# Optimization experiments

Measured on AMD Instinct MI355X. Metric: run time of the kernel, lower is better.

Reference implementation:

```python
import jax, jax.numpy as jnp
import numpy as np

N_GENES = 3072
N_CELLS = 3072
HIDDEN = 64
CAUSAL = 16
CS = 32
ALPHA = 0.35  # LeakyReLU negative slope
NEG_BIG = -9.0e15


def setup_inputs() -> dict:
    key = jax.random.key(0)
    ks = jax.random.split(key, 20)
    s = 0.05
    return {
        "x": jax.random.normal(ks[0], (N_CELLS, N_GENES), jnp.float32),
        "adj": jax.random.randint(ks[1], (N_GENES, N_GENES), 0, 2, jnp.int32),
        "eps": jax.random.normal(ks[2], (N_GENES, CAUSAL), jnp.float32),
        "W_gat": jax.random.normal(ks[3], (N_CELLS, HIDDEN), jnp.float32) * s,
        "a_gat": jax.random.normal(ks[4], (2 * HIDDEN,), jnp.float32) * s,
        "W_mu": jax.random.normal(ks[5], (HIDDEN, CAUSAL), jnp.float32) * s,
        "b_mu": jnp.zeros((CAUSAL,), jnp.float32),
        "W_lv": jax.random.normal(ks[6], (HIDDEN, CAUSAL), jnp.float32) * s,
        "b_lv": jnp.zeros((CAUSAL,), jnp.float32),
        "W_diff": jax.random.normal(ks[7], (CAUSAL + HIDDEN, CS), jnp.float32) * s,
        "b_diff": jnp.zeros((CS,), jnp.float32),
        "W_dec": jax.random.normal(ks[8], (CS, N_CELLS), jnp.float32) * s,
        "b_dec": jnp.zeros((N_CELLS,), jnp.float32),
        "W_gcn1": jax.random.normal(ks[9], (N_CELLS, HIDDEN), jnp.float32) * s,
        "W_gcn2": jax.random.normal(ks[10], (HIDDEN, HIDDEN), jnp.float32) * s,
    }


def _gcn(xg, adjf, W):
    # adj + I, symmetric normalization D^-1/2 A D^-1/2, then A_norm @ (x @ W), relu
    A = adjf + jnp.eye(adjf.shape[0], dtype=adjf.dtype)
    d = A.sum(axis=1)
    d_inv_sqrt = jnp.where(d > 0, d ** -0.5, 0.0)
    A_norm = d_inv_sqrt[:, None] * A * d_inv_sqrt[None, :]
    return jax.nn.relu(A_norm @ (xg @ W))


def reference(x, adj, eps, W_gat, a_gat, W_mu, b_mu, W_lv, b_lv,
              W_diff, b_diff, W_dec, b_dec, W_gcn1, W_gcn2):
    adjf = adj.astype(jnp.float32)
    # ---- GAT layer (batch of 1, squeezed). h: (M, F)
    h = x.T @ W_gat
    F = h.shape[1]
    # a_input[i, j] = concat(h_j, h_i)  => e_ij = leakyrelu(a1.h_j + a2.h_i)
    s_dst = h @ a_gat[:F]   # contribution of column index j
    s_src = h @ a_gat[F:]   # contribution of row index i
    e = jax.nn.leaky_relu(s_src[:, None] + s_dst[None, :], ALPHA)
    e = jnp.where(adjf > 0, e, NEG_BIG)
    att = jax.nn.softmax(e, axis=1)  # dropout p=0.1 is identity in eval mode
    h_gat = jax.nn.elu(att @ h)      # (M, HIDDEN)
    # ---- causal VAE encode + reparameterize
    mu = h_gat @ W_mu + b_mu
    logvar = h_gat @ W_lv + b_lv
    z = mu + eps * jnp.exp(0.5 * logvar)
    # ---- diffusion fusion
    cs = jax.nn.relu(jnp.concatenate([z, h_gat], axis=-1) @ W_diff + b_diff)
    # ---- decoder
    x_recon = jax.nn.sigmoid(cs @ W_dec + b_dec)  # (M, N_CELLS)
    # ---- inference model (two GCN layers on x_recon.T, as in original code)
    h1 = _gcn(x_recon.T, adjf, W_gcn1)
    h2 = _gcn(h1, adjf, W_gcn2)
    ie = jnp.concatenate([h2, cs], axis=-1)
    return (x_recon, h2, ie, cs, mu, logvar)
```

## Files before the change

kernel.cpp:

```cpp
#include <hip/hip_runtime.h>
#include <math.h>

#define N 3072
#define H 64
#define CAUS 16
#define CSD 32
#define GAT_ALPHA 0.35f
#define SLICES 8
#define JSL (N / SLICES)
#define MMS 16
#define JMM (N / MMS)
#define NH (N * H)
typedef unsigned long long u64;
typedef unsigned short u16;
typedef __attribute__((ext_vector_type(4))) float f32x4;
typedef __attribute__((ext_vector_type(8))) short s16x8;
struct alignas(8) u16x4 { u16 x, y, z, w; };
struct T4 { float4 r[4]; };

__device__ inline u16 f2bf(float f) {
  unsigned u = __builtin_bit_cast(unsigned, f);
  u += 0x7fffu + ((u >> 16) & 1u);
  return (u16)(u >> 16);
}

__device__ inline T4 t_load(const float* __restrict__ src, int ld, int t) {
  int k4 = (t >> 4) * 4, m4 = (t & 15) * 4;
  T4 o;
#pragma unroll
  for (int d = 0; d < 4; d++)
    o.r[d] = *(const float4*)(src + (size_t)(k4 + d) * ld + m4);
  return o;
}
__device__ inline void t_store(u16 (&dst)[64][72], const T4& v, int t) {
  int k4 = (t >> 4) * 4, m4 = (t & 15) * 4;
  u16x4 c0 = {f2bf(v.r[0].x), f2bf(v.r[1].x), f2bf(v.r[2].x), f2bf(v.r[3].x)};
  u16x4 c1 = {f2bf(v.r[0].y), f2bf(v.r[1].y), f2bf(v.r[2].y), f2bf(v.r[3].y)};
  u16x4 c2 = {f2bf(v.r[0].z), f2bf(v.r[1].z), f2bf(v.r[2].z), f2bf(v.r[3].z)};
  u16x4 c3 = {f2bf(v.r[0].w), f2bf(v.r[1].w), f2bf(v.r[2].w), f2bf(v.r[3].w)};
  *(u16x4*)&dst[m4 + 0][k4] = c0;
  *(u16x4*)&dst[m4 + 1][k4] = c1;
  *(u16x4*)&dst[m4 + 2][k4] = c2;
  *(u16x4*)&dst[m4 + 3][k4] = c3;
}

__global__ __launch_bounds__(256) void k_pack(const int* __restrict__ adj,
                                              u64* __restrict__ packed,
                                              float* __restrict__ dis) {
  int row = blockIdx.x * 4 + (threadIdx.x >> 6);
  int lane = threadIdx.x & 63;
  const int* ar = adj + (size_t)row * N;
  int deg = 0;
  for (int w0 = 0; w0 < 48; w0 += 8) {
    int vals[8];
#pragma unroll
    for (int q = 0; q < 8; q++) vals[q] = ar[(w0 + q) * 64 + lane];
#pragma unroll
    for (int q = 0; q < 8; q++) {
      u64 m = __ballot(vals[q] > 0);
      if (lane == 0) packed[(size_t)row * 48 + w0 + q] = m;
      deg += (vals[q] > 0) ? 1 : 0;
    }
  }
  for (int off = 32; off; off >>= 1) deg += __shfl_xor(deg, off);
  if (lane == 0) dis[row] = rsqrtf((float)deg + 1.0f);
}

__global__ __launch_bounds__(256) void k_mm32(const float* __restrict__ A, int lda,
                                              const float* __restrict__ B, int ldb,
                                              float* __restrict__ outp) {
  __shared__ u16 As[32][72];
  __shared__ u16 Bs[64][72];
  int t = threadIdx.x;
  int g0 = blockIdx.x * 32;
  int c0 = blockIdx.y * JMM;
  int w = t >> 6, l = t & 63, il = l & 15, kg = l >> 4;
  int ri = w & 1, cj = w >> 1;
  int ak = (t >> 3) * 2, am = (t & 7) * 4;
  f32x4 acc0 = {0.f, 0.f, 0.f, 0.f}, acc1 = {0.f, 0.f, 0.f, 0.f};
  float4 a0 = *(const float4*)(A + (size_t)(c0 + ak) * lda + g0 + am);
  float4 a1 = *(const float4*)(A + (size_t)(c0 + ak + 1) * lda + g0 + am);
  T4 bv = t_load(B + (size_t)c0 * ldb, ldb, t);
  for (int cb = 0; cb < JMM; cb += 64) {
    __syncthreads();
    As[am + 0][ak] = f2bf(a0.x); As[am + 1][ak] = f2bf(a0.y);
    As[am + 2][ak] = f2bf(a0.z); As[am + 3][ak] = f2bf(a0.w);
    As[am + 0][ak + 1] = f2bf(a1.x); As[am + 1][ak + 1] = f2bf(a1.y);
    As[am + 2][ak + 1] = f2bf(a1.z); As[am + 3][ak + 1] = f2bf(a1.w);
    t_store(Bs, bv, t);
    if (cb + 64 < JMM) {
      a0 = *(const float4*)(A + (size_t)(c0 + cb + 64 + ak) * lda + g0 + am);
      a1 = *(const float4*)(A + (size_t)(c0 + cb + 65 + ak) * lda + g0 + am);
      bv = t_load(B + (size_t)(c0 + cb + 64) * ldb, ldb, t);
    }
    __syncthreads();
#pragma unroll
    for (int kk = 0; kk < 64; kk += 32) {
      s16x8 a = *(const s16x8*)&As[ri * 16 + il][kk + kg * 8];
      s16x8 b0 = *(const s16x8*)&Bs[cj * 32 + il][kk + kg * 8];
      s16x8 b1 = *(const s16x8*)&Bs[cj * 32 + 16 + il][kk + kg * 8];
      acc0 = __builtin_amdgcn_mfma_f32_16x16x32_bf16(a, b0, acc0, 0, 0, 0);
      acc1 = __builtin_amdgcn_mfma_f32_16x16x32_bf16(a, b1, acc1, 0, 0, 0);
    }
  }
  float* ob = outp + (size_t)blockIdx.y * NH;
#pragma unroll
  for (int c = 0; c < 2; c++) {
    f32x4 acc = c ? acc1 : acc0;
    int col = cj * 32 + c * 16 + il;
    int rbase = g0 + ri * 16 + kg * 4;
#pragma unroll
    for (int r = 0; r < 4; r++)
      ob[(size_t)(rbase + r) * H + col] = acc[r];
  }
}

template <int GAT>
__global__ __launch_bounds__(256) void k_agg(const float* __restrict__ hin,
                                             const u64* __restrict__ packed,
                                             const float* __restrict__ sdst,
                                             const float* __restrict__ ssrc,
                                             const float* __restrict__ dis,
                                             float* __restrict__ outp,
                                             float* __restrict__ zpart) {
  __shared__ u16 Ws[32][72];
  __shared__ u16 Hs[64][72];
  __shared__ float ssl[32];
  int t = threadIdx.x;
  int i0 = blockIdx.x * 32;
  int jbase = blockIdx.y * JSL;
  int w = t >> 6, l = t & 63, il = l & 15, kg = l >> 4;
  int ri = w & 1, cj = w >> 1;
  int r = t >> 3, jq = (t & 7) * 8;
  if (GAT && t < 32) ssl[t] = ssrc[i0 + t];
  __syncthreads();
  float sv = GAT ? ssl[r] : 0.f;
  float zacc = 0.f;
  f32x4 acc0 = {0.f, 0.f, 0.f, 0.f}, acc1 = {0.f, 0.f, 0.f, 0.f};

  auto gen_w = [&](int j0, float (&wv)[8]) {
    u64 wb = packed[(size_t)(i0 + r) * 48 + (j0 >> 6)];
    if (GAT) {
      const float4* s4p = (const float4*)(sdst + j0 + jq);
      float4 s0 = s4p[0], s1 = s4p[1];
      float sf[8] = {s0.x, s0.y, s0.z, s0.w, s1.x, s1.y, s1.z, s1.w};
#pragma unroll
      for (int q = 0; q < 8; q++) {
        float e = sv + sf[q];
        e = e > 0.f ? e : GAT_ALPHA * e;
        float ww = ((wb >> (jq + q)) & 1ULL) ? __expf(e) : 0.f;
        wv[q] = ww;
        zacc += ww;
      }
    } else {
      const float4* d4p = (const float4*)(dis + j0 + jq);
      float4 d0 = d4p[0], d1 = d4p[1];
      float df[8] = {d0.x, d0.y, d0.z, d0.w, d1.x, d1.y, d1.z, d1.w};
#pragma unroll
      for (int q = 0; q < 8; q++) {
        float cnt = (float)((wb >> (jq + q)) & 1ULL) +
                    ((i0 + r) == (j0 + jq + q) ? 1.f : 0.f);
        wv[q] = cnt * df[q];
      }
    }
  };

  T4 hv = t_load(hin + (size_t)jbase * H, H, t);
  float wv[8];
  gen_w(jbase, wv);
  for (int jb = 0; jb < JSL; jb += 64) {
    __syncthreads();
    t_store(Hs, hv, t);
    u16x4 w0 = {f2bf(wv[0]), f2bf(wv[1]), f2bf(wv[2]), f2bf(wv[3])};
    u16x4 w1 = {f2bf(wv[4]), f2bf(wv[5]), f2bf(wv[6]), f2bf(wv[7])};
    *(u16x4*)&Ws[r][jq] = w0;
    *(u16x4*)&Ws[r][jq + 4] = w1;
    if (jb + 64 < JSL) {
      hv = t_load(hin + (size_t)(jbase + jb + 64) * H, H, t);
      gen_w(jbase + jb + 64, wv);
    }
    __syncthreads();
#pragma unroll
    for (int kk = 0; kk < 64; kk += 32) {
      s16x8 a = *(const s16x8*)&Ws[ri * 16 + il][kk + kg * 8];
      s16x8 b0 = *(const s16x8*)&Hs[cj * 32 + il][kk + kg * 8];
      s16x8 b1 = *(const s16x8*)&Hs[cj * 32 + 16 + il][kk + kg * 8];
      acc0 = __builtin_amdgcn_mfma_f32_16x16x32_bf16(a, b0, acc0, 0, 0, 0);
      acc1 = __builtin_amdgcn_mfma_f32_16x16x32_bf16(a, b1, acc1, 0, 0, 0);
    }
  }
  if (GAT) {
    zacc += __shfl_xor(zacc, 1);
    zacc += __shfl_xor(zacc, 2);
    zacc += __shfl_xor(zacc, 4);
    if ((t & 7) == 0) zpart[(size_t)blockIdx.y * N + i0 + r] = zacc;
  }
  float* ob = outp + (size_t)blockIdx.y * NH;
#pragma unroll
  for (int c = 0; c < 2; c++) {
    f32x4 acc = c ? acc1 : acc0;
    int col = cj * 32 + c * 16 + il;
    int rbase = i0 + ri * 16 + kg * 4;
#pragma unroll
    for (int rr = 0; rr < 4; rr++)
      ob[(size_t)(rbase + rr) * H + col] = acc[rr];
  }
}

__global__ __launch_bounds__(256) void k_mmdec32(const float* __restrict__ cs,
                                                 const float* __restrict__ Wdec,
                                                 const float* __restrict__ bdec,
                                                 const float* __restrict__ Wg1,
                                                 float* __restrict__ xr,
                                                 float* __restrict__ outp) {
  __shared__ u16 As[32][72];
  __shared__ u16 Bs[64][72];
  __shared__ u16 Wd[32][40];
  __shared__ u16 Csh[64][40];
  __shared__ float bs_s[32];
  int t = threadIdx.x;
  int g0 = blockIdx.x * 32;
  int c0 = blockIdx.y * JSL;
  int w = t >> 6, l = t & 63, il = l & 15, kg = l >> 4;
  int ri = w & 1, cj = w >> 1;
  {
    int q = t >> 3, m4 = (t & 7) * 4;
    float4 v = *(const float4*)(Wdec + (size_t)q * N + g0 + m4);
    Wd[m4 + 0][q] = f2bf(v.x); Wd[m4 + 1][q] = f2bf(v.y);
    Wd[m4 + 2][q] = f2bf(v.z); Wd[m4 + 3][q] = f2bf(v.w);
    if (t < 32) bs_s[t] = bdec[g0 + t];
  }
  int cell = t >> 3, qf = (t & 7) * 4;
  float4 cv0 = *(const float4*)(cs + (size_t)(c0 + cell) * CSD + qf);
  float4 cv1 = *(const float4*)(cs + (size_t)(c0 + 32 + cell) * CSD + qf);
  T4 bv = t_load(Wg1 + (size_t)c0 * H, H, t);
  f32x4 z = {0.f, 0.f, 0.f, 0.f};
  f32x4 acc0 = z, acc1 = z;
  for (int cb = 0; cb < JSL; cb += 64) {
    __syncthreads();
    u16x4 u0 = {f2bf(cv0.x), f2bf(cv0.y), f2bf(cv0.z), f2bf(cv0.w)};
    u16x4 u1 = {f2bf(cv1.x), f2bf(cv1.y), f2bf(cv1.z), f2bf(cv1.w)};
    *(u16x4*)&Csh[cell][qf] = u0;
    *(u16x4*)&Csh[cell + 32][qf] = u1;
    t_store(Bs, bv, t);
    if (cb + 64 < JSL) {
      cv0 = *(const float4*)(cs + (size_t)(c0 + cb + 64 + cell) * CSD + qf);
      cv1 = *(const float4*)(cs + (size_t)(c0 + cb + 96 + cell) * CSD + qf);
      bv = t_load(Wg1 + (size_t)(c0 + cb + 64) * H, H, t);
    }
    __syncthreads();
    f32x4 dec0 = z, dec1 = z;
    {
      s16x8 a = *(const s16x8*)&Wd[ri * 16 + il][kg * 8];
      s16x8 b0 = *(const s16x8*)&Csh[cj * 32 + il][kg * 8];
      s16x8 b1 = *(const s16x8*)&Csh[cj * 32 + 16 + il][kg * 8];
      dec0 = __builtin_amdgcn_mfma_f32_16x16x32_bf16(a, b0, dec0, 0, 0, 0);
      dec1 = __builtin_amdgcn_mfma_f32_16x16x32_bf16(a, b1, dec1, 0, 0, 0);
    }
#pragma unroll
    for (int c = 0; c < 2; c++) {
      f32x4 dv = c ? dec1 : dec0;
      int kcol = cj * 32 + c * 16 + il;
      int mb = ri * 16 + kg * 4;
      float4 sv4;
      float* sp = (float*)&sv4;
#pragma unroll
      for (int r = 0; r < 4; r++) {
        float pre = dv[r] + bs_s[mb + r];
        float sg = 1.f / (1.f + __expf(-pre));
        sp[r] = sg;
        As[mb + r][kcol] = f2bf(sg);
      }
      *(float4*)(xr + (size_t)(c0 + cb + kcol) * N + g0 + mb) = sv4;
    }
    __syncthreads();
#pragma unroll
    for (int kk = 0; kk < 64; kk += 32) {
      s16x8 a = *(const s16x8*)&As[ri * 16 + il][kk + kg * 8];
      s16x8 b0 = *(const s16x8*)&Bs[cj * 32 + il][kk + kg * 8];
      s16x8 b1 = *(const s16x8*)&Bs[cj * 32 + 16 + il][kk + kg * 8];
      acc0 = __builtin_amdgcn_mfma_f32_16x16x32_bf16(a, b0, acc0, 0, 0, 0);
      acc1 = __builtin_amdgcn_mfma_f32_16x16x32_bf16(a, b1, acc1, 0, 0, 0);
    }
  }
  float* ob = outp + (size_t)blockIdx.y * NH;
#pragma unroll
  for (int c = 0; c < 2; c++) {
    f32x4 acc = c ? acc1 : acc0;
    int col = cj * 32 + c * 16 + il;
    int rbase = g0 + ri * 16 + kg * 4;
#pragma unroll
    for (int r = 0; r < 4; r++)
      ob[(size_t)(rbase + r) * H + col] = acc[r];
  }
}

__global__ __launch_bounds__(256) void k_reduce_sd(const float* __restrict__ src,
                                                   const float* __restrict__ a,
                                                   float* __restrict__ h,
                                                   float* __restrict__ sdst,
                                                   float* __restrict__ ssrc) {
  int row = blockIdx.x * 4 + (threadIdx.x >> 6);
  int lane = threadIdx.x & 63;
  size_t off = (size_t)row * H + lane;
  float v = 0.f;
#pragma unroll
  for (int p = 0; p < MMS; p++) v += src[(size_t)p * NH + off];
  h[off] = v;
  float d1 = v * a[lane];
  float d2 = v * a[H + lane];
  for (int o = 32; o; o >>= 1) {
    d1 += __shfl_xor(d1, o);
    d2 += __shfl_xor(d2, o);
  }
  if (lane == 0) { sdst[row] = d1; ssrc[row] = d2; }
}

__global__ __launch_bounds__(256) void k_reduce(const float4* __restrict__ src,
                                                float4* __restrict__ dst) {
  int idx = blockIdx.x * 256 + threadIdx.x;
  float4 v = {0, 0, 0, 0};
#pragma unroll
  for (int p = 0; p < SLICES; p++) {
    float4 u = src[(size_t)p * (NH / 4) + idx];
    v.x += u.x; v.y += u.y; v.z += u.z; v.w += u.w;
  }
  dst[idx] = v;
}

__global__ __launch_bounds__(256) void k_vae(const float* __restrict__ hacc,
                                             const float* __restrict__ zpart,
                                             const float* __restrict__ eps,
                                             const float* __restrict__ Wmu,
                                             const float* __restrict__ bmu,
                                             const float* __restrict__ Wlv,
                                             const float* __restrict__ blv,
                                             const float* __restrict__ Wd,
                                             const float* __restrict__ bd,
                                             float* __restrict__ mu_o,
                                             float* __restrict__ lv_o,
                                             float* __restrict__ cs_o,
                                             float* __restrict__ ie) {
  __shared__ float hs[16][65];
  __shared__ float zs[16][17];
  __shared__ float wmu_s[1024];
  __shared__ float wlv_s[1024];
  __shared__ float wd_s[2560];
  int t = threadIdx.x;
  int row0 = blockIdx.x * 16;
  {
    int rr = t >> 4, pp = t & 15;
    float zv = (pp < SLICES) ? zpart[(size_t)pp * N + row0 + rr] : 0.f;
    zv += __shfl_xor(zv, 1);
    zv += __shfl_xor(zv, 2);
    zv += __shfl_xor(zv, 4);
    zv += __shfl_xor(zv, 8);
    float zi = 1.0f / fmaxf(zv, 1e-30f);
    const float4* g4 = (const float4*)(hacc + (size_t)row0 * H);
    float4 v = {0, 0, 0, 0};
#pragma unroll
    for (int p = 0; p < SLICES; p++) {
      float4 u = g4[(size_t)p * (NH / 4) + t];
      v.x += u.x; v.y += u.y; v.z += u.z; v.w += u.w;
    }
    int c0 = (t & 15) * 4;
    float e0 = v.x * zi, e1 = v.y * zi, e2 = v.z * zi, e3 = v.w * zi;
    hs[rr][c0 + 0] = e0 > 0.f ? e0 : __expf(e0) - 1.f;
    hs[rr][c0 + 1] = e1 > 0.f ? e1 : __expf(e1) - 1.f;
    hs[rr][c0 + 2] = e2 > 0.f ? e2 : __expf(e2) - 1.f;
    hs[rr][c0 + 3] = e3 > 0.f ? e3 : __expf(e3) - 1.f;
  }
#pragma unroll
  for (int k = 0; k < 4; k++) {
    int lin = t + k * 256;
    wmu_s[lin] = Wmu[lin];
    wlv_s[lin] = Wlv[lin];
  }
#pragma unroll
  for (int k = 0; k < 10; k++) {
    int lin = t + k * 256;
    wd_s[lin] = Wd[lin];
  }
  __syncthreads();
  int r = t >> 4, kk = t & 15;
  float mu = bmu[kk], lv = blv[kk];
#pragma unroll 8
  for (int l = 0; l < 64; l++) {
    float hv = hs[r][l];
    mu += hv * wmu_s[l * 16 + kk];
    lv += hv * wlv_s[l * 16 + kk];
  }
  float zc = mu + eps[(size_t)(row0 + r) * CAUS + kk] * __expf(0.5f * lv);
  mu_o[(size_t)(row0 + r) * CAUS + kk] = mu;
  lv_o[(size_t)(row0 + r) * CAUS + kk] = lv;
  zs[r][kk] = zc;
  __syncthreads();
#pragma unroll
  for (int p = 0; p < 2; p++) {
    int lin = t + p * 256;
    int rr = lin >> 5, c = lin & 31;
    float acc = bd[c];
#pragma unroll 4
    for (int q = 0; q < 16; q++) acc += zs[rr][q] * wd_s[q * 32 + c];
#pragma unroll 8
    for (int l = 0; l < 64; l++) acc += hs[rr][l] * wd_s[(16 + l) * 32 + c];
    float v = fmaxf(acc, 0.f);
    cs_o[(size_t)(row0 + rr) * CSD + c] = v;
    ie[(size_t)(row0 + rr) * 96 + 64 + c] = v;
  }
}

__global__ __launch_bounds__(256) void k_h1w2(const float* __restrict__ h1src,
                                              const float* __restrict__ dis,
                                              const float* __restrict__ W2,
                                              float* __restrict__ t2) {
  __shared__ float w2s[64 * 64];
  __shared__ float hs[4][65];
  int t = threadIdx.x;
  int row0 = blockIdx.x * 4;
#pragma unroll
  for (int k = 0; k < 16; k++) w2s[t + k * 256] = W2[t + k * 256];
  {
    int rr = t >> 6;
    size_t off = (size_t)row0 * H + t;
    float v = 0.f;
#pragma unroll
    for (int p = 0; p < SLICES; p++) v += h1src[(size_t)p * NH + off];
    hs[rr][t & 63] = fmaxf(v * dis[row0 + rr], 0.f);
  }
  __syncthreads();
  int r = t >> 6, f = t & 63;
  float acc = 0.f;
#pragma unroll 8
  for (int l = 0; l < 64; l++) acc += hs[r][l] * w2s[l * 64 + f];
  t2[(size_t)(row0 + r) * H + f] = acc;
}

__global__ __launch_bounds__(256) void k_fin2(const float* __restrict__ h2src,
                                              const float* __restrict__ dis,
                                              float* __restrict__ h2,
                                              float* __restrict__ ie) {
  int idx = blockIdx.x * 256 + threadIdx.x;
  int row = idx >> 6, f = idx & 63;
  float v = 0.f;
#pragma unroll
  for (int p = 0; p < SLICES; p++) v += h2src[(size_t)p * NH + idx];
  v = fmaxf(v * dis[row], 0.f);
  h2[idx] = v;
  ie[(size_t)row * 96 + f] = v;
}

extern "C" void kernel_launch(void* const* d_in, const int* in_sizes, int n_in,
                              void* d_out, int out_size, void* d_ws, size_t ws_size,
                              hipStream_t stream) {
  const float* x    = (const float*)d_in[0];
  const int*   adj  = (const int*)d_in[1];
  const float* eps  = (const float*)d_in[2];
  const float* Wgat = (const float*)d_in[3];
  const float* agat = (const float*)d_in[4];
  const float* Wmu  = (const float*)d_in[5];
  const float* bmu  = (const float*)d_in[6];
  const float* Wlv  = (const float*)d_in[7];
  const float* blv  = (const float*)d_in[8];
  const float* Wdif = (const float*)d_in[9];
  const float* bdif = (const float*)d_in[10];
  const float* Wdec = (const float*)d_in[11];
  const float* bdec = (const float*)d_in[12];
  const float* Wg1  = (const float*)d_in[13];
  const float* Wg2  = (const float*)d_in[14];

  float* out = (float*)d_out;
  float* xr  = out;
  float* h2  = out + 9437184;
  float* ie  = out + 9633792;
  float* cs  = out + 9928704;
  float* muo = out + 10027008;
  float* lvo = out + 10076160;

  u64* packed = (u64*)d_ws;
  float* wf    = (float*)d_ws + 294912;
  float* part  = wf;
  float* h     = part + (size_t)MMS * NH;
  float* t1    = h + NH;
  float* t2    = t1 + NH;
  float* sdst  = t2 + NH;
  float* ssrc  = sdst + N;
  float* dis   = ssrc + N;
  float* zpart = dis + N;

  k_mm32<<<dim3(96, MMS), 256, 0, stream>>>(x, N, Wgat, H, part);
  k_pack<<<768, 256, 0, stream>>>(adj, packed, dis);
  k_reduce_sd<<<768, 256, 0, stream>>>(part, agat, h, sdst, ssrc);
  k_agg<1><<<dim3(96, SLICES), 256, 0, stream>>>(h, packed, sdst, ssrc, dis,
                                                 part, zpart);
  k_vae<<<192, 256, 0, stream>>>(part, zpart, eps, Wmu, bmu, Wlv, blv,
                                 Wdif, bdif, muo, lvo, cs, ie);
  k_mmdec32<<<dim3(96, SLICES), 256, 0, stream>>>(cs, Wdec, bdec, Wg1, xr, part);
  k_reduce<<<192, 256, 0, stream>>>((const float4*)part, (float4*)t1);
  k_agg<0><<<dim3(96, SLICES), 256, 0, stream>>>(t1, packed, nullptr, nullptr,
                                                 dis, part, nullptr);
  k_h1w2<<<768, 256, 0, stream>>>(part, dis, Wg2, t2);
  k_agg<0><<<dim3(96, SLICES), 256, 0, stream>>>(t2, packed, nullptr, nullptr,
                                                 dis, part, nullptr);
  k_fin2<<<768, 256, 0, stream>>>(part, dis, h2, ie);
}
```

Baseline: 100.5 us.

## Fuse GAT projection with adjacency packing and split decoder over more slices

Merges the x^T@W_gat matmul and the adjacency bit-packing into one launch. Extra blocks beyond 1536 do the packing, which saves a launch and lets the two independent stages run at the same time. Both the matmul and the decoder kernel now load all three 64-deep K chunks up front instead of double-buffering one chunk. The decoder is split into 16 slices instead of 8, which gives it more blocks but doubles the partial buffers that k_reduce must sum. Together these raise register pressure and partial-sum traffic in exchange for more memory-level parallelism.

```diff
diff --git a/kernel.cpp b/kernel.cpp
--- a/kernel.cpp
+++ b/kernel.cpp
@@ -44,55 +44,56 @@
   *(u16x4*)&dst[m4 + 3][k4] = c3;
 }
 
-__global__ __launch_bounds__(256) void k_pack(const int* __restrict__ adj,
+__global__ __launch_bounds__(256) void k_mmpk(const float* __restrict__ x,
+                                              const float* __restrict__ Wgat,
+                                              float* __restrict__ part,
+                                              const int* __restrict__ adj,
                                               u64* __restrict__ packed,
                                               float* __restrict__ dis) {
-  int row = blockIdx.x * 4 + (threadIdx.x >> 6);
-  int lane = threadIdx.x & 63;
-  const int* ar = adj + (size_t)row * N;
-  int deg = 0;
-  for (int w0 = 0; w0 < 48; w0 += 8) {
-    int vals[8];
-#pragma unroll
-    for (int q = 0; q < 8; q++) vals[q] = ar[(w0 + q) * 64 + lane];
-#pragma unroll
-    for (int q = 0; q < 8; q++) {
-      u64 m = __ballot(vals[q] > 0);
-      if (lane == 0) packed[(size_t)row * 48 + w0 + q] = m;
-      deg += (vals[q] > 0) ? 1 : 0;
-    }
-  }
-  for (int off = 32; off; off >>= 1) deg += __shfl_xor(deg, off);
-  if (lane == 0) dis[row] = rsqrtf((float)deg + 1.0f);
-}
-
-__global__ __launch_bounds__(256) void k_mm32(const float* __restrict__ A, int lda,
-                                              const float* __restrict__ B, int ldb,
-                                              float* __restrict__ outp) {
   __shared__ u16 As[32][72];
   __shared__ u16 Bs[64][72];
-  int t = threadIdx.x;
-  int g0 = blockIdx.x * 32;
-  int c0 = blockIdx.y * JMM;
+  int bid = blockIdx.x, t = threadIdx.x;
+  if (bid >= 1536) {
+    int row = (bid - 1536) * 4 + (t >> 6), lane = t & 63;
+    const int* ar = adj + (size_t)row * N;
+    int deg = 0;
+    for (int w0 = 0; w0 < 48; w0 += 8) {
+      int vals[8];
+#pragma unroll
+      for (int q = 0; q < 8; q++) vals[q] = ar[(w0 + q) * 64 + lane];
+#pragma unroll
+      for (int q = 0; q < 8; q++) {
+        u64 m = __ballot(vals[q] > 0);
+        if (lane == 0) packed[(size_t)row * 48 + w0 + q] = m;
+        deg += (vals[q] > 0) ? 1 : 0;
+      }
+    }
+    for (int off = 32; off; off >>= 1) deg += __shfl_xor(deg, off);
+    if (lane == 0) dis[row] = rsqrtf((float)deg + 1.0f);
+    return;
+  }
+  int gx = bid % 96, sl = bid / 96;
+  int g0 = gx * 32, c0 = sl * JMM;
   int w = t >> 6, l = t & 63, il = l & 15, kg = l >> 4;
   int ri = w & 1, cj = w >> 1;
   int ak = (t >> 3) * 2, am = (t & 7) * 4;
+  float4 a0[3], a1[3];
+  T4 bv[3];
+#pragma unroll
+  for (int it = 0; it < 3; it++) {
+    a0[it] = *(const float4*)(x + (size_t)(c0 + it * 64 + ak) * N + g0 + am);
+    a1[it] = *(const float4*)(x + (size_t)(c0 + it * 64 + ak + 1) * N + g0 + am);
+    bv[it] = t_load(Wgat + (size_t)(c0 + it * 64) * H, H, t);
+  }
   f32x4 acc0 = {0.f, 0.f, 0.f, 0.f}, acc1 = {0.f, 0.f, 0.f, 0.f};
-  float4 a0 = *(const float4*)(A + (size_t)(c0 + ak) * lda + g0 + am);
-  float4 a1 = *(const float4*)(A + (size_t)(c0 + ak + 1) * lda + g0 + am);
-  T4 bv = t_load(B + (size_t)c0 * ldb, ldb, t);
-  for (int cb = 0; cb < JMM; cb += 64) {
-    __syncthreads();
-    As[am + 0][ak] = f2bf(a0.x); As[am + 1][ak] = f2bf(a0.y);
-    As[am + 2][ak] = f2bf(a0.z); As[am + 3][ak] = f2bf(a0.w);
-    As[am + 0][ak + 1] = f2bf(a1.x); As[am + 1][ak + 1] = f2bf(a1.y);
-    As[am + 2][ak + 1] = f2bf(a1.z); As[am + 3][ak + 1] = f2bf(a1.w);
-    t_store(Bs, bv, t);
-    if (cb + 64 < JMM) {
-      a0 = *(const float4*)(A + (size_t)(c0 + cb + 64 + ak) * lda + g0 + am);
-      a1 = *(const float4*)(A + (size_t)(c0 + cb + 65 + ak) * lda + g0 + am);
-      bv = t_load(B + (size_t)(c0 + cb + 64) * ldb, ldb, t);
-    }
+#pragma unroll
+  for (int it = 0; it < 3; it++) {
+    __syncthreads();
+    As[am + 0][ak] = f2bf(a0[it].x); As[am + 1][ak] = f2bf(a0[it].y);
+    As[am + 2][ak] = f2bf(a0[it].z); As[am + 3][ak] = f2bf(a0[it].w);
+    As[am + 0][ak + 1] = f2bf(a1[it].x); As[am + 1][ak + 1] = f2bf(a1[it].y);
+    As[am + 2][ak + 1] = f2bf(a1[it].z); As[am + 3][ak + 1] = f2bf(a1[it].w);
+    t_store(Bs, bv[it], t);
     __syncthreads();
 #pragma unroll
     for (int kk = 0; kk < 64; kk += 32) {
@@ -103,7 +104,7 @@
       acc1 = __builtin_amdgcn_mfma_f32_16x16x32_bf16(a, b1, acc1, 0, 0, 0);
     }
   }
-  float* ob = outp + (size_t)blockIdx.y * NH;
+  float* ob = part + (size_t)sl * NH;
 #pragma unroll
   for (int c = 0; c < 2; c++) {
     f32x4 acc = c ? acc1 : acc0;
@@ -207,12 +208,12 @@
   }
 }
 
-__global__ __launch_bounds__(256) void k_mmdec32(const float* __restrict__ cs,
-                                                 const float* __restrict__ Wdec,
-                                                 const float* __restrict__ bdec,
-                                                 const float* __restrict__ Wg1,
-                                                 float* __restrict__ xr,
-                                                 float* __restrict__ outp) {
+__global__ __launch_bounds__(256) void k_dec32(const float* __restrict__ cs,
+                                               const float* __restrict__ Wdec,
+                                               const float* __restrict__ bdec,
+                                               const float* __restrict__ Wg1,
+                                               float* __restrict__ xr,
+                                               float* __restrict__ outp) {
   __shared__ u16 As[32][72];
   __shared__ u16 Bs[64][72];
   __shared__ u16 Wd[32][40];
@@ -220,7 +221,7 @@
   __shared__ float bs_s[32];
   int t = threadIdx.x;
   int g0 = blockIdx.x * 32;
-  int c0 = blockIdx.y * JSL;
+  int c0 = blockIdx.y * JMM;
   int w = t >> 6, l = t & 63, il = l & 15, kg = l >> 4;
   int ri = w & 1, cj = w >> 1;
   {
@@ -231,23 +232,25 @@
     if (t < 32) bs_s[t] = bdec[g0 + t];
   }
   int cell = t >> 3, qf = (t & 7) * 4;
-  float4 cv0 = *(const float4*)(cs + (size_t)(c0 + cell) * CSD + qf);
-  float4 cv1 = *(const float4*)(cs + (size_t)(c0 + 32 + cell) * CSD + qf);
-  T4 bv = t_load(Wg1 + (size_t)c0 * H, H, t);
+  float4 cv0[3], cv1[3];
+  T4 bv[3];
+#pragma unroll
+  for (int it = 0; it < 3; it++) {
+    cv0[it] = *(const float4*)(cs + (size_t)(c0 + it * 64 + cell) * CSD + qf);
+    cv1[it] = *(const float4*)(cs + (size_t)(c0 + it * 64 + 32 + cell) * CSD + qf);
+    bv[it] = t_load(Wg1 + (size_t)(c0 + it * 64) * H, H, t);
+  }
   f32x4 z = {0.f, 0.f, 0.f, 0.f};
   f32x4 acc0 = z, acc1 = z;
-  for (int cb = 0; cb < JSL; cb += 64) {
-    __syncthreads();
-    u16x4 u0 = {f2bf(cv0.x), f2bf(cv0.y), f2bf(cv0.z), f2bf(cv0.w)};
-    u16x4 u1 = {f2bf(cv1.x), f2bf(cv1.y), f2bf(cv1.z), f2bf(cv1.w)};
+#pragma unroll
+  for (int it = 0; it < 3; it++) {
+    int cb = it * 64;
+    __syncthreads();
+    u16x4 u0 = {f2bf(cv0[it].x), f2bf(cv0[it].y), f2bf(cv0[it].z), f2bf(cv0[it].w)};
+    u16x4 u1 = {f2bf(cv1[it].x), f2bf(cv1[it].y), f2bf(cv1[it].z), f2bf(cv1[it].w)};
     *(u16x4*)&Csh[cell][qf] = u0;
     *(u16x4*)&Csh[cell + 32][qf] = u1;
-    t_store(Bs, bv, t);
-    if (cb + 64 < JSL) {
-      cv0 = *(const float4*)(cs + (size_t)(c0 + cb + 64 + cell) * CSD + qf);
-      cv1 = *(const float4*)(cs + (size_t)(c0 + cb + 96 + cell) * CSD + qf);
-      bv = t_load(Wg1 + (size_t)(c0 + cb + 64) * H, H, t);
-    }
+    t_store(Bs, bv[it], t);
     __syncthreads();
     f32x4 dec0 = z, dec1 = z;
     {
@@ -321,7 +324,7 @@
   int idx = blockIdx.x * 256 + threadIdx.x;
   float4 v = {0, 0, 0, 0};
 #pragma unroll
-  for (int p = 0; p < SLICES; p++) {
+  for (int p = 0; p < MMS; p++) {
     float4 u = src[(size_t)p * (NH / 4) + idx];
     v.x += u.x; v.y += u.y; v.z += u.z; v.w += u.w;
   }
@@ -488,14 +491,13 @@
   float* dis   = ssrc + N;
   float* zpart = dis + N;
 
-  k_mm32<<<dim3(96, MMS), 256, 0, stream>>>(x, N, Wgat, H, part);
-  k_pack<<<768, 256, 0, stream>>>(adj, packed, dis);
+  k_mmpk<<<2304, 256, 0, stream>>>(x, Wgat, part, adj, packed, dis);
   k_reduce_sd<<<768, 256, 0, stream>>>(part, agat, h, sdst, ssrc);
   k_agg<1><<<dim3(96, SLICES), 256, 0, stream>>>(h, packed, sdst, ssrc, dis,
                                                  part, zpart);
   k_vae<<<192, 256, 0, stream>>>(part, zpart, eps, Wmu, bmu, Wlv, blv,
                                  Wdif, bdif, muo, lvo, cs, ie);
-  k_mmdec32<<<dim3(96, SLICES), 256, 0, stream>>>(cs, Wdec, bdec, Wg1, xr, part);
+  k_dec32<<<dim3(96, MMS), 256, 0, stream>>>(cs, Wdec, bdec, Wg1, xr, part);
   k_reduce<<<192, 256, 0, stream>>>((const float4*)part, (float4*)t1);
   k_agg<0><<<dim3(96, SLICES), 256, 0, stream>>>(t1, packed, nullptr, nullptr,
                                                  dis, part, nullptr);
```

New measurement: 99.35 us, median of 2. Within noise of the previous version (-1.1%).
